# Kernel optimization log

Hardware: AMD Instinct MI355X
Metric: run time of the kernel (lower is better)

Reference implementation:

```python
import jax, jax.numpy as jnp
import numpy as np
import math

NUM_HEADS = 16

def get_slopes(n):
    def pow2(n):
        start = 2 ** (-2 ** (-(math.log2(n) - 3)))
        return [start * start ** i for i in range(n)]
    if math.log2(n).is_integer():
        return pow2(n)
    c = 2 ** math.floor(math.log2(n))
    return pow2(c) + get_slopes(2 * c)[0::2][: n - c]


def setup_inputs() -> dict:
    key = jax.random.key(0)
    ks = jax.random.split(key, 5)
    B, T, C = 2, 2048, 1024
    return {
        "x": jax.random.normal(ks[0], (B, T, C), dtype=jnp.float32),
        "W_qkv": jax.random.normal(ks[1], (C, 3 * C), dtype=jnp.float32) * 0.02,
        "b_qkv": jax.random.normal(ks[2], (3 * C,), dtype=jnp.float32) * 0.02,
        "W_proj": jax.random.normal(ks[3], (C, C), dtype=jnp.float32) * 0.02,
        "b_proj": jax.random.normal(ks[4], (C,), dtype=jnp.float32) * 0.02,
    }


def reference(x, W_qkv, b_qkv, W_proj, b_proj):
    B, T, C = x.shape
    H = NUM_HEADS
    D = C // H
    qkv = x @ W_qkv + b_qkv                       # [B,T,3C]
    q, k, v = jnp.split(qkv, 3, axis=-1)
    q = q.reshape(B, T, H, D).transpose(0, 2, 1, 3)  # [B,H,T,D]
    k = k.reshape(B, T, H, D).transpose(0, 2, 1, 3)
    v = v.reshape(B, T, H, D).transpose(0, 2, 1, 3)

    slopes = jnp.asarray(get_slopes(H), dtype=jnp.float32)  # [H]
    idx = jnp.arange(T)
    # alibi_bias(L).T in source: -(i-j) for j<=i, 0 for j>i  == min(j-i, 0)
    alibi = jnp.minimum(idx[None, :] - idx[:, None], 0).astype(jnp.float32)  # [T,T]
    bias = slopes[:, None, None] * alibi          # [H,T,T]

    scale = 1.0 / math.sqrt(D)
    scores = jnp.einsum("bhtd,bhsd->bhts", q, k) * scale + bias[None]
    # NOTE: source code builds a causal -inf mask but never adds it -> non-causal
    w = jax.nn.softmax(scores, axis=-1)
    y = jnp.einsum("bhts,bhsd->bhtd", w, v)       # [B,H,T,D]
    y = y.transpose(0, 2, 1, 3).reshape(B, T, C)
    return y @ W_proj + b_proj
```

## Files before the change

kernel.cpp:

```cpp
#include <hip/hip_runtime.h>
#include <hip/hip_bf16.h>
#include <cmath>
#include <cstdint>

typedef __bf16 bf16_t;
typedef __bf16 bf16x8 __attribute__((ext_vector_type(8)));
typedef float f32x4 __attribute__((ext_vector_type(4)));
typedef float f32x8 __attribute__((ext_vector_type(8)));

static_assert(sizeof(bf16x8) == 16, "bf16x8 must be 16B");

#define MFMA16(a, b, c) __builtin_amdgcn_mfma_f32_16x16x32_bf16((a), (b), (c), 0, 0, 0)

__global__ void detect_dtype(const unsigned short* __restrict__ x,
                             int* __restrict__ flag) {
  const int lane = threadIdx.x;
  int cnt = 0;
#pragma unroll
  for (int t = 0; t < 8; ++t) {
    unsigned short u = x[2 * (lane + 64 * t)];
    int e = (u >> 7) & 0xFF;
    cnt += (e >= 90 && e <= 130) ? 1 : 0;
  }
#pragma unroll
  for (int off = 1; off < 64; off <<= 1) cnt += __shfl_xor(cnt, off, 64);
  if (lane == 0) *flag = (cnt < 300) ? 1 : 0;
}

__global__ __launch_bounds__(256) void convert_x(const void* __restrict__ x_,
                                                 bf16_t* __restrict__ xb,
                                                 const int* __restrict__ flagp) {
  const size_t idx = ((size_t)blockIdx.x * 256 + threadIdx.x) * 8;
  if (*flagp) {
    f32x8 v = *(const f32x8*)((const float*)x_ + idx);
    bf16x8 bv;
#pragma unroll
    for (int e = 0; e < 8; ++e) bv[e] = (bf16_t)v[e];
    *(bf16x8*)&xb[idx] = bv;
  } else {
    *(bf16x8*)&xb[idx] = *(const bf16x8*)((const bf16_t*)x_ + idx);
  }
}

__global__ __launch_bounds__(256) void wt_transpose(const void* __restrict__ W_,
                                                    bf16_t* __restrict__ Wt,
                                                    int K, int N,
                                                    const int* __restrict__ flagp) {
  __shared__ bf16_t tile[64 * 72];
  const int is_f32 = *flagp;
  const int tid = threadIdx.x;
  const int k0 = blockIdx.y * 64;
  const int n0 = blockIdx.x * 64;
  const int r = tid >> 3;
  const int c = (tid & 7) * 8;
#pragma unroll
  for (int t = 0; t < 2; ++t) {
    int rr = r + t * 32;
    if (is_f32) {
      const float* W = (const float*)W_;
      f32x8 v = *(const f32x8*)&W[(size_t)(k0 + rr) * N + n0 + c];
      bf16x8 bv;
#pragma unroll
      for (int e = 0; e < 8; ++e) bv[e] = (bf16_t)v[e];
      *(bf16x8*)&tile[rr * 72 + c] = bv;
    } else {
      const bf16_t* W = (const bf16_t*)W_;
      *(bf16x8*)&tile[rr * 72 + c] = *(const bf16x8*)&W[(size_t)(k0 + rr) * N + n0 + c];
    }
  }
  __syncthreads();
#pragma unroll
  for (int t = 0; t < 2; ++t) {
    int rr = r + t * 32;
    bf16x8 v;
#pragma unroll
    for (int e = 0; e < 8; ++e) v[e] = tile[(c + e) * 72 + rr];
    *(bf16x8*)&Wt[(size_t)(n0 + rr) * K + k0 + c] = v;
  }
}

__global__ __launch_bounds__(256, 2) void gemm_bt(
    const bf16_t* __restrict__ A, const bf16_t* __restrict__ Bt,
    const void* __restrict__ bias_, void* __restrict__ C_,
    bf16_t* __restrict__ qb, bf16_t* __restrict__ kb, bf16_t* __restrict__ vt,
    int M, int N, int K, int mode, const int* __restrict__ flagp) {
  __shared__ bf16_t As[128 * 72];
  __shared__ bf16_t Bs[128 * 72];
  const int is_f32 = *flagp;
  const int tid = threadIdx.x;
  const int wave = tid >> 6, lane = tid & 63;
  const int l16 = lane & 15, quad = lane >> 4;
  const int m0 = blockIdx.y * 128, n0 = blockIdx.x * 128;
  const int wm = (wave >> 1) * 64, wn = (wave & 1) * 64;
  f32x4 acc[4][4] = {};

  for (int k0 = 0; k0 < K; k0 += 64) {
#pragma unroll
    for (int t = 0; t < 4; ++t) {
      int ch = tid + t * 256;
      int r = ch >> 3, c = (ch & 7) * 8;
      *(bf16x8*)&As[r * 72 + c] = *(const bf16x8*)&A[(size_t)(m0 + r) * K + k0 + c];
      *(bf16x8*)&Bs[r * 72 + c] = *(const bf16x8*)&Bt[(size_t)(n0 + r) * K + k0 + c];
    }
    __syncthreads();
#pragma unroll
    for (int ks = 0; ks < 2; ++ks) {
      bf16x8 af[4], bfr[4];
#pragma unroll
      for (int i = 0; i < 4; ++i) {
        af[i]  = *(const bf16x8*)&As[(wm + i * 16 + l16) * 72 + ks * 32 + quad * 8];
        bfr[i] = *(const bf16x8*)&Bs[(wn + i * 16 + l16) * 72 + ks * 32 + quad * 8];
      }
#pragma unroll
      for (int i = 0; i < 4; ++i)
#pragma unroll
        for (int j = 0; j < 4; ++j)
          acc[i][j] = MFMA16(af[i], bfr[j], acc[i][j]);
    }
    __syncthreads();
  }

#pragma unroll
  for (int j = 0; j < 4; ++j) {
    const int n = n0 + wn + j * 16 + l16;
    const float bv = is_f32 ? ((const float*)bias_)[n]
                            : (float)((const bf16_t*)bias_)[n];
    if (mode == 0) {
#pragma unroll
      for (int i = 0; i < 4; ++i)
#pragma unroll
        for (int r = 0; r < 4; ++r) {
          int m = m0 + wm + i * 16 + quad * 4 + r;
          float val = acc[i][j][r] + bv;
          if (is_f32) ((float*)C_)[(size_t)m * N + n] = val;
          else ((bf16_t*)C_)[(size_t)m * N + n] = (bf16_t)val;
        }
    } else {
      const int region = n >> 10;
      const int nn = n & 1023;
      const int hh = nn >> 6, dd = nn & 63;
#pragma unroll
      for (int i = 0; i < 4; ++i)
#pragma unroll
        for (int r = 0; r < 4; ++r) {
          int m = m0 + wm + i * 16 + quad * 4 + r;
          int bb = m >> 11, tt = m & 2047;
          size_t bh = (size_t)(bb * 16 + hh);
          float val = acc[i][j][r] + bv;
          if (region == 0)
            qb[(bh * 2048 + tt) * 64 + dd] = (bf16_t)val;
          else if (region == 1)
            kb[(bh * 2048 + tt) * 64 + dd] = (bf16_t)val;
          else
            vt[bh * 131072 + (size_t)dd * 2048 + tt] = (bf16_t)val;
        }
    }
  }
}

__global__ __launch_bounds__(256, 2) void attn_kernel(
    const bf16_t* __restrict__ qbuf, const bf16_t* __restrict__ kbuf,
    const bf16_t* __restrict__ vT, bf16_t* __restrict__ y) {
  const int T = 2048;
  __shared__ bf16_t Ks[64 * 72];
  __shared__ bf16_t VTs[64 * 72];
  __shared__ bf16_t Ps[4][32 * 72];

  const int tid = threadIdx.x;
  const int wave = tid >> 6, lane = tid & 63;
  const int l16 = lane & 15, quad = lane >> 4;
  const int bh = blockIdx.y;
  const int b = bh >> 4, h = bh & 15;
  const int i0 = blockIdx.x * 128 + wave * 32;
  const float L2E = 1.44269504088896f;
  const float c1 = 0.125f * L2E;
  const float c2 = exp2f(-0.5f * (float)(h + 1)) * L2E;

  bf16x8 qf[2][2];
#pragma unroll
  for (int g = 0; g < 2; ++g) {
    const bf16_t* qrow = qbuf + ((size_t)bh * T + i0 + g * 16 + l16) * 64;
    qf[g][0] = *(const bf16x8*)&qrow[quad * 8];
    qf[g][1] = *(const bf16x8*)&qrow[32 + quad * 8];
  }

  f32x4 o[2][4] = {};
  float rsum[2][4] = {};

  const bf16_t* kbase = kbuf + (size_t)bh * T * 64;
  const bf16_t* vbase = vT + (size_t)bh * 64 * T;

  const int sr = tid >> 3, sc = (tid & 7) * 8;

  for (int j0 = 0; j0 < T; j0 += 64) {
#pragma unroll
    for (int t = 0; t < 2; ++t) {
      int rr = sr + t * 32;
      *(bf16x8*)&Ks[rr * 72 + sc] = *(const bf16x8*)&kbase[(size_t)(j0 + rr) * 64 + sc];
      *(bf16x8*)&VTs[rr * 72 + sc] = *(const bf16x8*)&vbase[(size_t)rr * T + j0 + sc];
    }
    __syncthreads();

    bf16x8 kf[4][2];
#pragma unroll
    for (int jt = 0; jt < 4; ++jt) {
      kf[jt][0] = *(const bf16x8*)&Ks[(jt * 16 + l16) * 72 + quad * 8];
      kf[jt][1] = *(const bf16x8*)&Ks[(jt * 16 + l16) * 72 + 32 + quad * 8];
    }

    bf16_t* Pw = Ps[wave];
    const float jb = (float)(j0 + l16);
#pragma unroll
    for (int g = 0; g < 2; ++g) {
      f32x4 s[4] = {};
#pragma unroll
      for (int jt = 0; jt < 4; ++jt) {
        s[jt] = MFMA16(qf[g][0], kf[jt][0], s[jt]);
        s[jt] = MFMA16(qf[g][1], kf[jt][1], s[jt]);
      }
      const float fb = (float)(i0 + g * 16 + quad * 4);
#pragma unroll
      for (int jt = 0; jt < 4; ++jt) {
        const float jmf = jb + (float)(16 * jt);
#pragma unroll
        for (int r = 0; r < 4; ++r) {
          float dm = fminf(jmf - (fb + (float)r), 0.0f);
          float p = exp2f(c1 * s[jt][r] + c2 * dm);
          rsum[g][r] += p;
          Pw[(g * 16 + quad * 4 + r) * 72 + jt * 16 + l16] = (bf16_t)p;
        }
      }
    }
    __asm__ volatile("s_waitcnt lgkmcnt(0)" ::: "memory");

    bf16x8 vf[4][2];
#pragma unroll
    for (int dt = 0; dt < 4; ++dt) {
      vf[dt][0] = *(const bf16x8*)&VTs[(dt * 16 + l16) * 72 + quad * 8];
      vf[dt][1] = *(const bf16x8*)&VTs[(dt * 16 + l16) * 72 + 32 + quad * 8];
    }
#pragma unroll
    for (int g = 0; g < 2; ++g) {
      const bf16x8 pf0 = *(const bf16x8*)&Pw[(g * 16 + l16) * 72 + quad * 8];
      const bf16x8 pf1 = *(const bf16x8*)&Pw[(g * 16 + l16) * 72 + 32 + quad * 8];
#pragma unroll
      for (int dt = 0; dt < 4; ++dt) {
        o[g][dt] = MFMA16(pf0, vf[dt][0], o[g][dt]);
        o[g][dt] = MFMA16(pf1, vf[dt][1], o[g][dt]);
      }
    }
    __syncthreads();
  }

#pragma unroll
  for (int g = 0; g < 2; ++g)
#pragma unroll
    for (int r = 0; r < 4; ++r) {
      float s = rsum[g][r];
      s += __shfl_xor(s, 1, 64);
      s += __shfl_xor(s, 2, 64);
      s += __shfl_xor(s, 4, 64);
      s += __shfl_xor(s, 8, 64);
      rsum[g][r] = s;
    }

#pragma unroll
  for (int g = 0; g < 2; ++g)
#pragma unroll
    for (int dt = 0; dt < 4; ++dt)
#pragma unroll
      for (int r = 0; r < 4; ++r) {
        const int ig = i0 + g * 16 + quad * 4 + r;
        const int d = dt * 16 + l16;
        y[((size_t)(b * 2048 + ig)) * 1024 + h * 64 + d] =
            (bf16_t)(o[g][dt][r] / rsum[g][r]);
      }
}

extern "C" void kernel_launch(void* const* d_in, const int* in_sizes, int n_in,
                              void* d_out, int out_size, void* d_ws, size_t ws_size,
                              hipStream_t stream) {
  const void* x     = d_in[0];
  const void* Wqkv  = d_in[1];
  const void* bqkv  = d_in[2];
  const void* Wproj = d_in[3];
  const void* bproj = d_in[4];

  const size_t SEG = (size_t)32 * 2048 * 64;
  bf16_t* ws = (bf16_t*)d_ws;
  bf16_t* qb = ws;
  bf16_t* kb = ws + SEG;
  bf16_t* vt = ws + 2 * SEG;
  bf16_t* yb = ws + 3 * SEG;
  bf16_t* WqkvT  = yb;
  bf16_t* WprojT = qb;
  bf16_t* xb = (bf16_t*)d_out;
  int* flag1 = (int*)((char*)d_ws + (size_t)31 * 1024 * 1024);
  int* flag2 = (int*)((char*)d_ws + (size_t)4 * 1024 * 1024);

  detect_dtype<<<1, 64, 0, stream>>>((const unsigned short*)x, flag1);
  wt_transpose<<<dim3(48, 16), 256, 0, stream>>>(Wqkv, WqkvT, 1024, 3072, flag1);
  convert_x<<<2048, 256, 0, stream>>>(x, xb, flag1);
  gemm_bt<<<dim3(24, 32), 256, 0, stream>>>(xb, WqkvT, bqkv, nullptr, qb, kb, vt,
                                            4096, 3072, 1024, 1, flag1);
  attn_kernel<<<dim3(16, 32), 256, 0, stream>>>(qb, kb, vt, yb);
  detect_dtype<<<1, 64, 0, stream>>>((const unsigned short*)x, flag2);
  wt_transpose<<<dim3(16, 16), 256, 0, stream>>>(Wproj, WprojT, 1024, 1024, flag2);
  gemm_bt<<<dim3(8, 32), 256, 0, stream>>>(yb, WprojT, bproj, d_out,
                                           nullptr, nullptr, nullptr,
                                           4096, 1024, 1024, 0, flag2);
}
```

Measured before the change: 260.7 us.

## Split attention key range across two wave groups and use direct-to-LDS loads in GEMM

The attention kernel now runs 512 threads per block, with two groups of four waves each processing half of the key sequence for the same query rows. Partial outputs and row sums are merged through shared memory at the end, and P is staged in smaller 32-column halves. This doubles the number of waves in flight, which should hide more latency, at the cost of a final cross-group reduction and more LDS per block. Separately, the GEMM stages tiles with global_load_lds directly into unpadded LDS, skipping register round-trips but possibly adding LDS bank conflicts on fragment reads.

```diff
diff --git a/kernel.cpp b/kernel.cpp
--- a/kernel.cpp
+++ b/kernel.cpp
@@ -11,6 +11,12 @@
 static_assert(sizeof(bf16x8) == 16, "bf16x8 must be 16B");
 
 #define MFMA16(a, b, c) __builtin_amdgcn_mfma_f32_16x16x32_bf16((a), (b), (c), 0, 0, 0)
+
+__device__ __forceinline__ void load_lds_16B(const bf16_t* gsrc, bf16_t* ldst) {
+  __builtin_amdgcn_global_load_lds(
+      (const __attribute__((address_space(1))) void*)gsrc,
+      (__attribute__((address_space(3))) void*)ldst, 16, 0, 0);
+}
 
 __global__ void detect_dtype(const unsigned short* __restrict__ x,
                              int* __restrict__ flag) {
@@ -84,23 +90,24 @@
     const void* __restrict__ bias_, void* __restrict__ C_,
     bf16_t* __restrict__ qb, bf16_t* __restrict__ kb, bf16_t* __restrict__ vt,
     int M, int N, int K, int mode, const int* __restrict__ flagp) {
-  __shared__ bf16_t As[128 * 72];
-  __shared__ bf16_t Bs[128 * 72];
+  __shared__ bf16_t As[128 * 64];
+  __shared__ bf16_t Bs[128 * 64];
   const int is_f32 = *flagp;
   const int tid = threadIdx.x;
   const int wave = tid >> 6, lane = tid & 63;
   const int l16 = lane & 15, quad = lane >> 4;
   const int m0 = blockIdx.y * 128, n0 = blockIdx.x * 128;
   const int wm = (wave >> 1) * 64, wn = (wave & 1) * 64;
+  const int lr = lane >> 3, lc = (lane & 7) * 8;
   f32x4 acc[4][4] = {};
 
   for (int k0 = 0; k0 < K; k0 += 64) {
 #pragma unroll
     for (int t = 0; t < 4; ++t) {
-      int ch = tid + t * 256;
-      int r = ch >> 3, c = (ch & 7) * 8;
-      *(bf16x8*)&As[r * 72 + c] = *(const bf16x8*)&A[(size_t)(m0 + r) * K + k0 + c];
-      *(bf16x8*)&Bs[r * 72 + c] = *(const bf16x8*)&Bt[(size_t)(n0 + r) * K + k0 + c];
+      const int chunk = wave * 4 + t;
+      const int row = chunk * 8 + lr;
+      load_lds_16B(&A[(size_t)(m0 + row) * K + k0 + lc], &As[chunk * 512]);
+      load_lds_16B(&Bt[(size_t)(n0 + row) * K + k0 + lc], &Bs[chunk * 512]);
     }
     __syncthreads();
 #pragma unroll
@@ -108,8 +115,8 @@
       bf16x8 af[4], bfr[4];
 #pragma unroll
       for (int i = 0; i < 4; ++i) {
-        af[i]  = *(const bf16x8*)&As[(wm + i * 16 + l16) * 72 + ks * 32 + quad * 8];
-        bfr[i] = *(const bf16x8*)&Bs[(wn + i * 16 + l16) * 72 + ks * 32 + quad * 8];
+        af[i]  = *(const bf16x8*)&As[(wm + i * 16 + l16) * 64 + ks * 32 + quad * 8];
+        bfr[i] = *(const bf16x8*)&Bs[(wn + i * 16 + l16) * 64 + ks * 32 + quad * 8];
       }
 #pragma unroll
       for (int i = 0; i < 4; ++i)
@@ -158,20 +165,22 @@
   }
 }
 
-__global__ __launch_bounds__(256, 2) void attn_kernel(
+__global__ __launch_bounds__(512, 4) void attn_kernel(
     const bf16_t* __restrict__ qbuf, const bf16_t* __restrict__ kbuf,
     const bf16_t* __restrict__ vT, bf16_t* __restrict__ y) {
   const int T = 2048;
-  __shared__ bf16_t Ks[64 * 72];
-  __shared__ bf16_t VTs[64 * 72];
-  __shared__ bf16_t Ps[4][32 * 72];
+  __shared__ __align__(16) char smem[57344];
+  bf16_t* Ks  = (bf16_t*)smem;
+  bf16_t* VTs = (bf16_t*)(smem + 18432);
+  bf16_t* Ps  = (bf16_t*)(smem + 36864);
 
   const int tid = threadIdx.x;
   const int wave = tid >> 6, lane = tid & 63;
+  const int g2 = wave >> 2, wp = wave & 3;
   const int l16 = lane & 15, quad = lane >> 4;
   const int bh = blockIdx.y;
   const int b = bh >> 4, h = bh & 15;
-  const int i0 = blockIdx.x * 128 + wave * 32;
+  const int i0 = blockIdx.x * 128 + wp * 32;
   const float L2E = 1.44269504088896f;
   const float c1 = 0.125f * L2E;
   const float c2 = exp2f(-0.5f * (float)(h + 1)) * L2E;
@@ -190,63 +199,66 @@
   const bf16_t* kbase = kbuf + (size_t)bh * T * 64;
   const bf16_t* vbase = vT + (size_t)bh * 64 * T;
 
-  const int sr = tid >> 3, sc = (tid & 7) * 8;
-
-  for (int j0 = 0; j0 < T; j0 += 64) {
+  bf16_t* myKs = Ks + g2 * 4608;
+  bf16_t* myVs = VTs + g2 * 4608;
+  bf16_t* Pw = Ps + wave * 1280;
+
+  const int gtid = tid & 255;
+  const int sr = gtid >> 3, sc = (gtid & 7) * 8;
+  const int jbase = g2 * 1024;
+
+  for (int jj = 0; jj < 1024; jj += 64) {
+    const int j0 = jbase + jj;
 #pragma unroll
     for (int t = 0; t < 2; ++t) {
       int rr = sr + t * 32;
-      *(bf16x8*)&Ks[rr * 72 + sc] = *(const bf16x8*)&kbase[(size_t)(j0 + rr) * 64 + sc];
-      *(bf16x8*)&VTs[rr * 72 + sc] = *(const bf16x8*)&vbase[(size_t)rr * T + j0 + sc];
+      *(bf16x8*)&myKs[rr * 72 + sc] = *(const bf16x8*)&kbase[(size_t)(j0 + rr) * 64 + sc];
+      *(bf16x8*)&myVs[rr * 72 + sc] = *(const bf16x8*)&vbase[(size_t)rr * T + j0 + sc];
     }
     __syncthreads();
 
-    bf16x8 kf[4][2];
-#pragma unroll
-    for (int jt = 0; jt < 4; ++jt) {
-      kf[jt][0] = *(const bf16x8*)&Ks[(jt * 16 + l16) * 72 + quad * 8];
-      kf[jt][1] = *(const bf16x8*)&Ks[(jt * 16 + l16) * 72 + 32 + quad * 8];
-    }
-
-    bf16_t* Pw = Ps[wave];
-    const float jb = (float)(j0 + l16);
-#pragma unroll
-    for (int g = 0; g < 2; ++g) {
-      f32x4 s[4] = {};
-#pragma unroll
-      for (int jt = 0; jt < 4; ++jt) {
-        s[jt] = MFMA16(qf[g][0], kf[jt][0], s[jt]);
-        s[jt] = MFMA16(qf[g][1], kf[jt][1], s[jt]);
+#pragma unroll
+    for (int hl = 0; hl < 2; ++hl) {
+      bf16x8 kf[2][2];
+#pragma unroll
+      for (int jtl = 0; jtl < 2; ++jtl) {
+        const int jr = (hl * 2 + jtl) * 16 + l16;
+        kf[jtl][0] = *(const bf16x8*)&myKs[jr * 72 + quad * 8];
+        kf[jtl][1] = *(const bf16x8*)&myKs[jr * 72 + 32 + quad * 8];
       }
-      const float fb = (float)(i0 + g * 16 + quad * 4);
-#pragma unroll
-      for (int jt = 0; jt < 4; ++jt) {
-        const float jmf = jb + (float)(16 * jt);
-#pragma unroll
-        for (int r = 0; r < 4; ++r) {
-          float dm = fminf(jmf - (fb + (float)r), 0.0f);
-          float p = exp2f(c1 * s[jt][r] + c2 * dm);
-          rsum[g][r] += p;
-          Pw[(g * 16 + quad * 4 + r) * 72 + jt * 16 + l16] = (bf16_t)p;
+#pragma unroll
+      for (int g = 0; g < 2; ++g) {
+        f32x4 s[2] = {};
+#pragma unroll
+        for (int jtl = 0; jtl < 2; ++jtl) {
+          s[jtl] = MFMA16(qf[g][0], kf[jtl][0], s[jtl]);
+          s[jtl] = MFMA16(qf[g][1], kf[jtl][1], s[jtl]);
+        }
+        const float fb = (float)(i0 + g * 16 + quad * 4);
+#pragma unroll
+        for (int jtl = 0; jtl < 2; ++jtl) {
+          const float jmf = (float)(j0 + (hl * 2 + jtl) * 16 + l16);
+#pragma unroll
+          for (int r = 0; r < 4; ++r) {
+            float dm = fminf(jmf - (fb + (float)r), 0.0f);
+            float p = exp2f(c1 * s[jtl][r] + c2 * dm);
+            rsum[g][r] += p;
+            Pw[(g * 16 + quad * 4 + r) * 40 + jtl * 16 + l16] = (bf16_t)p;
+          }
         }
       }
-    }
-    __asm__ volatile("s_waitcnt lgkmcnt(0)" ::: "memory");
-
-    bf16x8 vf[4][2];
-#pragma unroll
-    for (int dt = 0; dt < 4; ++dt) {
-      vf[dt][0] = *(const bf16x8*)&VTs[(dt * 16 + l16) * 72 + quad * 8];
-      vf[dt][1] = *(const bf16x8*)&VTs[(dt * 16 + l16) * 72 + 32 + quad * 8];
-    }
-#pragma unroll
-    for (int g = 0; g < 2; ++g) {
-      const bf16x8 pf0 = *(const bf16x8*)&Pw[(g * 16 + l16) * 72 + quad * 8];
-      const bf16x8 pf1 = *(const bf16x8*)&Pw[(g * 16 + l16) * 72 + 32 + quad * 8];
-#pragma unroll
-      for (int dt = 0; dt < 4; ++dt) {
-        o[g][dt] = MFMA16(pf0, vf[dt][0], o[g][dt]);
-        o[g][dt] = MFMA16(pf1, vf[dt][1], o[g][dt]);
+      __asm__ volatile("s_waitcnt lgkmcnt(0)" ::: "memory");
+
+      bf16x8 vf[4];
+#pragma unroll
+      for (int dt = 0; dt < 4; ++dt)
+        vf[dt] = *(const bf16x8*)&myVs[(dt * 16 + l16) * 72 + hl * 32 + quad * 8];
+#pragma unroll
+      for (int g = 0; g < 2; ++g) {
+        const bf16x8 pf = *(const bf16x8*)&Pw[(g * 16 + l16) * 40 + quad * 8];
+#pragma unroll
+        for (int dt = 0; dt < 4; ++dt)
+          o[g][dt] = MFMA16(pf, vf[dt], o[g][dt]);
       }
     }
     __syncthreads();
@@ -264,17 +276,43 @@
       rsum[g][r] = s;
     }
 
-#pragma unroll
-  for (int g = 0; g < 2; ++g)
-#pragma unroll
-    for (int dt = 0; dt < 4; ++dt)
-#pragma unroll
-      for (int r = 0; r < 4; ++r) {
-        const int ig = i0 + g * 16 + quad * 4 + r;
-        const int d = dt * 16 + l16;
-        y[((size_t)(b * 2048 + ig)) * 1024 + h * 64 + d] =
-            (bf16_t)(o[g][dt][r] / rsum[g][r]);
-      }
+  __syncthreads();
+  float* exO = (float*)smem;
+  float* exR = (float*)(smem + 36864);
+  if (g2 == 1) {
+    float* myO = exO + wp * (32 * 65);
+#pragma unroll
+    for (int g = 0; g < 2; ++g)
+#pragma unroll
+      for (int dt = 0; dt < 4; ++dt)
+#pragma unroll
+        for (int r = 0; r < 4; ++r)
+          myO[(g * 16 + quad * 4 + r) * 65 + dt * 16 + l16] = o[g][dt][r];
+    if (l16 == 0) {
+#pragma unroll
+      for (int g = 0; g < 2; ++g)
+#pragma unroll
+        for (int r = 0; r < 4; ++r)
+          exR[wp * 32 + g * 16 + quad * 4 + r] = rsum[g][r];
+    }
+  }
+  __syncthreads();
+  if (g2 == 0) {
+    float* myO = exO + wp * (32 * 65);
+#pragma unroll
+    for (int g = 0; g < 2; ++g)
+#pragma unroll
+      for (int dt = 0; dt < 4; ++dt)
+#pragma unroll
+        for (int r = 0; r < 4; ++r) {
+          const int row = g * 16 + quad * 4 + r;
+          const float denom = rsum[g][r] + exR[wp * 32 + row];
+          const float val = (o[g][dt][r] + myO[row * 65 + dt * 16 + l16]) / denom;
+          const int ig = i0 + row;
+          const int d = dt * 16 + l16;
+          y[((size_t)(b * 2048 + ig)) * 1024 + h * 64 + d] = (bf16_t)val;
+        }
+  }
 }
 
 extern "C" void kernel_launch(void* const* d_in, const int* in_sizes, int n_in,
@@ -303,7 +341,7 @@
   convert_x<<<2048, 256, 0, stream>>>(x, xb, flag1);
   gemm_bt<<<dim3(24, 32), 256, 0, stream>>>(xb, WqkvT, bqkv, nullptr, qb, kb, vt,
                                             4096, 3072, 1024, 1, flag1);
-  attn_kernel<<<dim3(16, 32), 256, 0, stream>>>(qb, kb, vt, yb);
+  attn_kernel<<<dim3(16, 32), 512, 0, stream>>>(qb, kb, vt, yb);
   detect_dtype<<<1, 64, 0, stream>>>((const unsigned short*)x, flag2);
   wt_transpose<<<dim3(16, 16), 256, 0, stream>>>(Wproj, WprojT, 1024, 1024, flag2);
   gemm_bt<<<dim3(8, 32), 256, 0, stream>>>(yb, WprojT, bproj, d_out,
```

Measured after the change: 250.6 us. -3.9%, faster.
